# Performance work log

Hardware: AMD Instinct MI355X
Metric: run time of the kernel (lower is better)

Reference implementation:

```python
import jax, jax.numpy as jnp
import numpy as np

H = 1024      # hidden_dim
NH = 16       # num_heads
HD = H // NH  # head_dim
FF = 4096     # ff_dim
EPS = 1e-6


def layer_norm(x, gamma, beta):
    # faithful to source: unbiased std (ddof=1), divide by (std + eps)
    mean = jnp.mean(x, axis=-1, keepdims=True)
    var = jnp.sum((x - mean) ** 2, axis=-1, keepdims=True) / (x.shape[-1] - 1)
    std = jnp.sqrt(var)
    return gamma * (x - mean) / (std + EPS) + beta


def linear_mulbias(x, W, b):
    # source LinearLayer: einsum('...i,io,o->...o') -> (x @ W) * b (bias MULTIPLIES)
    return jnp.einsum('bti,io->bto', x, W) * b


def setup_inputs() -> dict:
    key = jax.random.key(0)
    ks = jax.random.split(key, 11)
    B, T = 2, 2048
    return {
        'x':      jax.random.normal(ks[0], (B, T, H), jnp.float32),
        'Wqkv':   jax.random.normal(ks[1], (H, 3 * H), jnp.float32),
        'bqkv':   jax.random.normal(ks[2], (3 * H,), jnp.float32),
        'W1':     jax.random.normal(ks[3], (H, FF), jnp.float32),
        'b1':     jax.random.normal(ks[4], (FF,), jnp.float32),
        'W2':     jax.random.normal(ks[5], (FF, H), jnp.float32),
        'b2':     jax.random.normal(ks[6], (H,), jnp.float32),
        'gamma1': jax.random.normal(ks[7], (H,), jnp.float32),
        'beta1':  jax.random.normal(ks[8], (H,), jnp.float32),
        'gamma2': jax.random.normal(ks[9], (H,), jnp.float32),
        'beta2':  jax.random.normal(ks[10], (H,), jnp.float32),
    }


def attention(x, Wqkv, bqkv):
    B, T, _ = x.shape
    qkv = linear_mulbias(x, Wqkv, bqkv)                 # [B,T,3H]
    # einops 'b t (d k h) -> k b h t d' with k=3, h=NH: last dim decomposes (d,3,h)
    qkv = qkv.reshape(B, T, HD, 3, NH)
    qkv = jnp.transpose(qkv, (3, 0, 4, 1, 2))           # [3,B,NH,T,HD]
    q, k, v = qkv[0], qkv[1], qkv[2]
    scores = jnp.einsum('bhid,bhjd->bhij', q, k) / (H ** 0.5)  # scale by full hidden_dim
    attn = jax.nn.softmax(scores, axis=-1)
    out = jnp.einsum('bhij,bhjd->bhid', attn, v)        # [B,NH,T,HD]
    return jnp.transpose(out, (0, 2, 1, 3)).reshape(B, T, H)


def reference(x, Wqkv, bqkv, W1, b1, W2, b2, gamma1, beta1, gamma2, beta2):
    # dropout is identity in eval mode
    out = layer_norm(x + attention(x, Wqkv, bqkv), gamma1, beta1)
    ffn = linear_mulbias(jnp.maximum(linear_mulbias(out, W1, b1), 0.0), W2, b2)
    out = layer_norm(out + ffn, gamma2, beta2)
    return out
```

## Files before the change

kernel.cpp:

```cpp
#include <hip/hip_runtime.h>
#include <math.h>

#define B 2
#define T 2048
#define H 1024
#define NH 16
#define HD 64
#define FF 4096
#define M_TOK (B*T)
#define LOG2E 1.4426950408889634f

typedef unsigned short u16;
typedef __attribute__((ext_vector_type(8))) short bf16x8;
typedef __attribute__((ext_vector_type(4))) float f32x4;

#define WAITBAR3  asm volatile("s_waitcnt vmcnt(3)\n\ts_barrier" ::: "memory")
#define WAITBAR4  asm volatile("s_waitcnt vmcnt(4)\n\ts_barrier" ::: "memory")
#define WAITBAR0  asm volatile("s_waitcnt vmcnt(0)\n\ts_barrier" ::: "memory")

__device__ __forceinline__ u16 f2bf(float f) {
  union { float f; unsigned u; } v; v.f = f;
  const unsigned r = (v.u + 0x7FFFu + ((v.u >> 16) & 1u)) >> 16;
  return (u16)r;
}
__device__ __forceinline__ float bf2f(u16 h) {
  union { unsigned u; float f; } v; v.u = ((unsigned)h) << 16;
  return v.f;
}
__device__ __forceinline__ unsigned cvt_pk_bf16(float lo, float hi) {
  unsigned r;
  asm("v_cvt_pk_bf16_f32 %0, %1, %2" : "=v"(r) : "v"(lo), "v"(hi));
  return r;
}
__device__ __forceinline__ float m3(float a, float b, float c) {
  return fmaxf(fmaxf(a, b), c);
}
__device__ __forceinline__ void gload16(const u16* g, u16* l) {
  __builtin_amdgcn_global_load_lds(
      (const __attribute__((address_space(1))) unsigned int*)g,
      (__attribute__((address_space(3))) unsigned int*)l, 16, 0, 0);
}

__device__ __forceinline__ int colperm(int c) {
  const int d = c / 48;
  const int rem = c - d * 48;
  return ((rem >> 4) << 10) | ((rem & 15) << 6) | d;
}

__global__ __launch_bounds__(256) void preprocess(
    const float* __restrict__ x, u16* __restrict__ xh, u16* __restrict__ xl,
    const float* __restrict__ Wqkv, u16* __restrict__ WqTh, u16* __restrict__ WqTl,
    const float* __restrict__ W1_, u16* __restrict__ W1T_,
    const float* __restrict__ W2_, u16* __restrict__ W2T_,
    const float* __restrict__ bqkv, float* __restrict__ bqkvP)
{
  const int bid = blockIdx.x;
  const int tid = threadIdx.x;
  if (bid == 6912) {
#pragma unroll
    for (int it = 0; it < 12; ++it) {
      const int c = it * 256 + tid;
      bqkvP[colperm(c)] = bqkv[c];
    }
    return;
  }
  if (bid < 4096) {
    const size_t i = ((size_t)bid * 256 + tid) * 4;
    const float4 v = *(const float4*)(x + i);
    union { u16 s[4]; uint2 u; } h, l;
    const float f[4] = {v.x, v.y, v.z, v.w};
#pragma unroll
    for (int j = 0; j < 4; ++j) {
      const u16 hb = f2bf(f[j]); h.s[j] = hb; l.s[j] = f2bf(f[j] - bf2f(hb));
    }
    *(uint2*)(xh + i) = h.u;
    *(uint2*)(xl + i) = l.u;
    return;
  }
  __shared__ float tile[64][69];
  const float* in; u16* oh; u16* ol = nullptr;
  int K, N, k0, n0, split = 0, permq = 0;
  if (bid < 4864) {
    const int tb = bid - 4096;
    in = Wqkv; oh = WqTh; ol = WqTl; K = H; N = 3*H; split = 1; permq = 1;
    n0 = (tb % 48) * 64; k0 = (tb / 48) * 64;
  } else if (bid < 5888) {
    const int tb = bid - 4864;
    in = W1_; oh = W1T_; K = H; N = FF;
    n0 = (tb & 63) * 64; k0 = (tb >> 6) * 64;
  } else {
    const int tb = bid - 5888;
    in = W2_; oh = W2T_; K = FF; N = H;
    n0 = (tb & 15) * 64; k0 = (tb >> 4) * 64;
  }
  const int r = tid >> 4, c4 = (tid & 15) * 4;
#pragma unroll
  for (int i = 0; i < 4; ++i) {
    const float4 v = *(const float4*)(in + (size_t)(k0 + i*16 + r) * N + n0 + c4);
    tile[i*16+r][c4]   = v.x; tile[i*16+r][c4+1] = v.y;
    tile[i*16+r][c4+2] = v.z; tile[i*16+r][c4+3] = v.w;
  }
  __syncthreads();
  const int n = tid >> 2, kq = tid & 3;
  union { u16 s[8]; int4 v; } ph0, ph1, pl0, pl1;
#pragma unroll
  for (int j = 0; j < 8; ++j) {
    const float f0 = tile[kq*16 + j][n];
    const float f1 = tile[kq*16 + 8 + j][n];
    const u16 h0 = f2bf(f0), h1 = f2bf(f1);
    ph0.s[j] = h0; ph1.s[j] = h1;
    if (split) { pl0.s[j] = f2bf(f0 - bf2f(h0)); pl1.s[j] = f2bf(f1 - bf2f(h1)); }
  }
  int orow = n0 + n;
  if (permq) orow = colperm(orow);
  u16* po = oh + (size_t)orow * K + k0 + kq * 16;
  *(int4*)po = ph0.v; *(int4*)(po + 8) = ph1.v;
  if (split) {
    u16* pl = ol + (size_t)orow * K + k0 + kq * 16;
    *(int4*)pl = pl0.v; *(int4*)(pl + 8) = pl1.v;
  }
}

__device__ __forceinline__ int swz(int r, int kq) {
  return r * 32 + ((kq ^ ((r >> 1) & 3)) * 8);
}

template<int RELU, int OBF>
__global__ __launch_bounds__(256) void mfma_gemm(
    const u16* __restrict__ Ah, const u16* __restrict__ Bh,
    const float* __restrict__ bias,
    float* __restrict__ Cf, u16* __restrict__ Cb,
    int M, int N, int K)
{
  __shared__ u16 lds[24576];
  const int tid = threadIdx.x;
  const int bid = blockIdx.x;
  const int xcd = bid & 7;
  const int idx = bid >> 3;
  const int row0 = (xcd * 4 + (idx & 3)) * 128;
  const int col0 = (idx >> 2) * 128;
  const int wv = tid >> 6, lane = tid & 63;
  const int wr = wv >> 1, wc = wv & 1;
  const int kq = lane >> 4, fr = lane & 15;

  f32x4 acc[4][4] = {};

#define GSTAGE(lbase, gb, rowbase, kk) do { \
    _Pragma("unroll") \
    for (int t_ = 0; t_ < 2; ++t_) { \
      const int c_ = wv * 2 + t_; \
      const int idx_ = c_ * 64 + lane; \
      const int r_ = idx_ >> 2; \
      const int kq_ = (idx_ & 3) ^ ((r_ >> 1) & 3); \
      gload16((gb) + (size_t)((rowbase) + r_) * K + (kk) + kq_ * 8, \
              &lds[(lbase) + c_ * 512]); \
    } } while (0)

  const int nk = K >> 5;
  GSTAGE(0, Ah, row0, 0);            GSTAGE(4096, Bh, col0, 0);
  GSTAGE(8192, Ah, row0, 32);        GSTAGE(8192 + 4096, Bh, col0, 32);
  WAITBAR4;
  int cslot = 0, islot = 2;
  for (int i = 0; i < nk; ++i) {
    if (i + 2 < nk) {
      const int kk = (i + 2) * 32;
      GSTAGE(islot * 8192, Ah, row0, kk);
      GSTAGE(islot * 8192 + 4096, Bh, col0, kk);
      islot = (islot == 2) ? 0 : islot + 1;
    }
    const int rb = cslot * 8192;
    bf16x8 a_h[4];
#pragma unroll
    for (int m = 0; m < 4; ++m)
      a_h[m] = *(const bf16x8*)&lds[rb + swz(wr*64 + m*16 + fr, kq)];
#pragma unroll
    for (int n = 0; n < 4; ++n) {
      const bf16x8 b_h = *(const bf16x8*)&lds[rb + 4096 + swz(wc*64 + n*16 + fr, kq)];
#pragma unroll
      for (int m = 0; m < 4; ++m)
        acc[m][n] = __builtin_amdgcn_mfma_f32_16x16x32_bf16(a_h[m], b_h, acc[m][n], 0, 0, 0);
    }
    cslot = (cslot == 2) ? 0 : cslot + 1;
    if (i + 1 < nk) { if (i + 2 < nk) WAITBAR4; else WAITBAR0; }
  }
#undef GSTAGE

  const int orow0 = row0 + wr * 64, ocol0 = col0 + wc * 64;
#pragma unroll
  for (int n = 0; n < 4; ++n) {
    const int col = ocol0 + n * 16 + fr;
    const float bs = bias[col];
#pragma unroll
    for (int m = 0; m < 4; ++m) {
      const int rbase = orow0 + m * 16 + kq * 4;
#pragma unroll
      for (int j = 0; j < 4; ++j) {
        float v = acc[m][n][j] * bs;
        if (RELU) v = fmaxf(v, 0.0f);
        const size_t off = (size_t)(rbase + j) * N + col;
        if (OBF) Cb[off] = f2bf(v); else Cf[off] = v;
      }
    }
  }
}

__global__ __launch_bounds__(256) void mfma_qkv(
    const u16* __restrict__ Ah, const u16* __restrict__ Al,
    const u16* __restrict__ Bh, const u16* __restrict__ Bl,
    const float* __restrict__ biasP,
    u16* __restrict__ Qh, u16* __restrict__ Ql,
    u16* __restrict__ Kh, u16* __restrict__ Kl, u16* __restrict__ VT)
{
  const int K = H;
  __shared__ u16 lds[32768];
  const int tid = threadIdx.x;
  const int bid = blockIdx.x;
  const int xcd = bid & 7;
  const int idx = bid >> 3;
  const int row0 = (xcd * 4 + (idx & 3)) * 128;
  const int col0 = (idx >> 2) * 128;
  const int wv = tid >> 6, lane = tid & 63;
  const int wr = wv >> 1, wc = wv & 1;
  const int kq = lane >> 4, fr = lane & 15;
  const bool isV = (col0 >= 2048);

  f32x4 acc[4][4] = {};

#define QSTAGE(lbase, gb, rowbase, kk) do { \
    _Pragma("unroll") \
    for (int t_ = 0; t_ < 2; ++t_) { \
      const int c_ = wv * 2 + t_; \
      const int idx_ = c_ * 64 + lane; \
      const int r_ = idx_ >> 2; \
      const int kq_ = (idx_ & 3) ^ ((r_ >> 1) & 3); \
      gload16((gb) + (size_t)((rowbase) + r_) * K + (kk) + kq_ * 8, \
              &lds[(lbase) + c_ * 512]); \
    } } while (0)

  QSTAGE(0, Ah, row0, 0);
  QSTAGE(4096, Bh, col0, 0);
  if (!isV) { QSTAGE(8192, Al, row0, 0); QSTAGE(12288, Bl, col0, 0); }
  __syncthreads();

  int cur = 0;
  for (int k0 = 0; k0 < K; k0 += 32) {
    const int nxt = cur ^ 1;
    if (k0 + 32 < K) {
      QSTAGE(nxt*16384, Ah, row0, k0 + 32);
      QSTAGE(nxt*16384 + 4096, Bh, col0, k0 + 32);
      if (!isV) { QSTAGE(nxt*16384 + 8192, Al, row0, k0 + 32);
                  QSTAGE(nxt*16384 + 12288, Bl, col0, k0 + 32); }
    }
    const int rb = cur * 16384;
    bf16x8 a_h[4], a_l[4];
#pragma unroll
    for (int m = 0; m < 4; ++m) {
      a_h[m] = *(const bf16x8*)&lds[rb + swz(wr*64 + m*16 + fr, kq)];
      if (!isV) a_l[m] = *(const bf16x8*)&lds[rb + 8192 + swz(wr*64 + m*16 + fr, kq)];
    }
#pragma unroll
    for (int n = 0; n < 4; ++n) {
      const bf16x8 b_h = *(const bf16x8*)&lds[rb + 4096 + swz(wc*64 + n*16 + fr, kq)];
#pragma unroll
      for (int m = 0; m < 4; ++m)
        acc[m][n] = __builtin_amdgcn_mfma_f32_16x16x32_bf16(a_h[m], b_h, acc[m][n], 0, 0, 0);
      if (!isV) {
        const bf16x8 b_l = *(const bf16x8*)&lds[rb + 12288 + swz(wc*64 + n*16 + fr, kq)];
#pragma unroll
        for (int m = 0; m < 4; ++m) {
          acc[m][n] = __builtin_amdgcn_mfma_f32_16x16x32_bf16(a_h[m], b_l, acc[m][n], 0, 0, 0);
          acc[m][n] = __builtin_amdgcn_mfma_f32_16x16x32_bf16(a_l[m], b_h, acc[m][n], 0, 0, 0);
        }
      }
    }
    __syncthreads();
    cur = nxt;
  }
#undef QSTAGE

  const float qscale = LOG2E / 32.0f;
  const int orow0 = row0 + wr * 64, ocol0 = col0 + wc * 64;
  const int kcls = col0 >> 10;

  if (kcls == 2) {
#pragma unroll
    for (int n = 0; n < 4; ++n) {
      const int dc = wc * 64 + n * 16 + fr;
      const float bs = biasP[ocol0 + n * 16 + fr];
#pragma unroll
      for (int m = 0; m < 4; ++m) {
        const int trb = wr * 64 + m * 16 + kq * 4;
#pragma unroll
        for (int j = 0; j < 4; ++j)
          lds[dc * 132 + trb + j] = f2bf(acc[m][n][j] * bs);
      }
    }
    __syncthreads();
    const int dr_ = tid >> 1, half = tid & 1;
    const int hh = ((col0 >> 6) & 15) + (dr_ >> 6);
    const int d = dr_ & 63;
    const int b = row0 >> 11, t0r = row0 & (T - 1);
    u16* dstp = VT + (((size_t)(b * NH + hh)) * HD + d) * T + t0r + half * 64;
    const int sbase = dr_ * 132 + half * 64;
#pragma unroll
    for (int q = 0; q < 8; ++q) {
      union { uint2 u2[2]; int4 v; } pkv;
      pkv.u2[0] = *(const uint2*)&lds[sbase + q * 8];
      pkv.u2[1] = *(const uint2*)&lds[sbase + q * 8 + 4];
      *(int4*)(dstp + q * 8) = pkv.v;
    }
    return;
  }

#pragma unroll
  for (int n = 0; n < 4; ++n) {
    const int colp = ocol0 + n * 16 + fr;
    const int d = colp & 63, hh = (colp >> 6) & 15;
    const float bs = biasP[colp];
#pragma unroll
    for (int m = 0; m < 4; ++m) {
      const int rbase = orow0 + m * 16 + kq * 4;
#pragma unroll
      for (int j = 0; j < 4; ++j) {
        const int row = rbase + j;
        const int b = row >> 11, t = row & (T - 1);
        const size_t dst = (((size_t)(b * NH + hh)) * T + t) * HD + d;
        float v = acc[m][n][j] * bs;
        if (kcls == 0) {
          v *= qscale;
          const u16 hb = f2bf(v);
          Qh[dst] = hb; Ql[dst] = f2bf(v - bf2f(hb));
        } else {
          const u16 hb = f2bf(v);
          Kh[dst] = hb; Kl[dst] = f2bf(v - bf2f(hb));
        }
      }
    }
  }
}

__global__ __launch_bounds__(512, 2) void mfma_ffn2(
    const u16* __restrict__ Ah, const u16* __restrict__ Bh,
    const u16* __restrict__ Res, const float* __restrict__ bias,
    float* __restrict__ Y)
{
  const int N = H, K = FF;
  __shared__ u16 lds[2 * 24576];
  const int tid = threadIdx.x;
  const int bid = blockIdx.x;
  const int xcd = bid & 7;
  const int idx = bid >> 3;
  const int row0 = (xcd * 4 + (idx & 3)) * 128;
  const int col0 = (idx >> 2) * 128;
  const int wv8 = tid >> 6, lane = tid & 63;
  const int grp = wv8 >> 2, wv = wv8 & 3;
  const int wr = wv >> 1, wc = wv & 1;
  const int kq = lane >> 4, fr = lane & 15;
  const int kb = grp * (K >> 1);
  u16* gl = &lds[grp * 24576];

  f32x4 acc[4][4] = {};

#define GSTAGE2(lbase, gb, rowbase, kk) do { \
    _Pragma("unroll") \
    for (int t_ = 0; t_ < 2; ++t_) { \
      const int c_ = wv * 2 + t_; \
      const int idx_ = c_ * 64 + lane; \
      const int r_ = idx_ >> 2; \
      const int kq_ = (idx_ & 3) ^ ((r_ >> 1) & 3); \
      gload16((gb) + (size_t)((rowbase) + r_) * K + (kk) + kq_ * 8, \
              &gl[(lbase) + c_ * 512]); \
    } } while (0)

  const int nk = (K >> 1) >> 5;
  GSTAGE2(0, Ah, row0, kb);            GSTAGE2(4096, Bh, col0, kb);
  GSTAGE2(8192, Ah, row0, kb + 32);    GSTAGE2(8192 + 4096, Bh, col0, kb + 32);
  WAITBAR4;
  int cslot = 0, islot = 2;
  for (int i = 0; i < nk; ++i) {
    if (i + 2 < nk) {
      const int kk = kb + (i + 2) * 32;
      GSTAGE2(islot * 8192, Ah, row0, kk);
      GSTAGE2(islot * 8192 + 4096, Bh, col0, kk);
      islot = (islot == 2) ? 0 : islot + 1;
    }
    const int rb = cslot * 8192;
    bf16x8 a_h[4];
#pragma unroll
    for (int m = 0; m < 4; ++m)
      a_h[m] = *(const bf16x8*)&gl[rb + swz(wr*64 + m*16 + fr, kq)];
#pragma unroll
    for (int n = 0; n < 4; ++n) {
      const bf16x8 b_h = *(const bf16x8*)&gl[rb + 4096 + swz(wc*64 + n*16 + fr, kq)];
#pragma unroll
      for (int m = 0; m < 4; ++m)
        acc[m][n] = __builtin_amdgcn_mfma_f32_16x16x32_bf16(a_h[m], b_h, acc[m][n], 0, 0, 0);
    }
    cslot = (cslot == 2) ? 0 : cslot + 1;
    if (i + 1 < nk) { if (i + 2 < nk) WAITBAR4; else WAITBAR0; }
  }
#undef GSTAGE2

  __syncthreads();
  float* fm = (float*)lds;
  const int base = wv * 4096;
  if (grp == 1) {
#pragma unroll
    for (int m = 0; m < 4; ++m)
#pragma unroll
      for (int n = 0; n < 4; ++n)
        *(f32x4*)&fm[base + (m*4 + n)*256 + lane*4] = acc[m][n];
  }
  __syncthreads();
  if (grp == 0) {
    const int orow0 = row0 + wr * 64, ocol0 = col0 + wc * 64;
#pragma unroll
    for (int n = 0; n < 4; ++n) {
      const int col = ocol0 + n * 16 + fr;
      const float bs = bias[col];
#pragma unroll
      for (int m = 0; m < 4; ++m) {
        const f32x4 ob = *(const f32x4*)&fm[base + (m*4 + n)*256 + lane*4];
        const int rbase = orow0 + m * 16 + kq * 4;
#pragma unroll
        for (int j = 0; j < 4; ++j) {
          const size_t off = (size_t)(rbase + j) * N + col;
          Y[off] = bf2f(Res[off]) + (acc[m][n][j] + ob[j]) * bs;
        }
      }
    }
  }
}

__device__ __forceinline__ int sigma_k(int r) {
  return ((r >> 5) << 5) | (((r >> 2) & 3) << 3) | (((r >> 4) & 1) << 2) | (r & 3);
}

__global__ __launch_bounds__(512, 4) void flash_attn_mfma(
    const u16* __restrict__ Qh, const u16* __restrict__ Ql,
    const u16* __restrict__ Kh, const u16* __restrict__ Kl,
    const u16* __restrict__ VT, float* __restrict__ Out)
{
  __shared__ u16 sm[3 * 12288];
  const int i = blockIdx.x;
  const int slot = i >> 3;
  const int bh = (i & 7) * 4 + (slot >> 4);
  const int row0 = (slot & 15) * 128;
  const int b = bh >> 4, h = bh & 15;
  const int tid = threadIdx.x, wave = tid >> 6, lane = tid & 63;
  const int fr = lane & 15, kq = lane >> 4;

  bf16x8 qh[2], ql[2];
  const size_t qoff = ((size_t)bh * T + row0 + wave*16 + fr) * HD + kq*8;
#pragma unroll
  for (int ks = 0; ks < 2; ++ks) {
    qh[ks] = *(const bf16x8*)(Qh + qoff + ks*32);
    ql[ks] = *(const bf16x8*)(Ql + qoff + ks*32);
  }

  bf16x8 ones8;
#pragma unroll
  for (int z = 0; z < 8; ++z) ones8[z] = (short)0x3F80;

  f32x4 o[4] = {};
  f32x4 oex = {};
  float m_ = -1e30f;

  const int c_ = wave;
  const int r0_ = c_ * 8 + (lane >> 3), s_ = lane & 7;
  const int cd0 = s_ ^ (r0_ & 7);
  const int k0_ = sigma_k(r0_);
  const u16* pKh0 = Kh + ((size_t)bh*T + k0_)*HD + cd0*8;
  const u16* pKl0 = Kl + ((size_t)bh*T + k0_)*HD + cd0*8;
  const u16* pV0  = VT + ((size_t)bh*HD + r0_)*T + cd0*8;

#define FSTAGE(sb) do { \
    gload16(pKh0, &sm[(sb) + c_*512]); \
    gload16(pKl0, &sm[(sb) + 4096 + c_*512]); \
    gload16(pV0,  &sm[(sb) + 8192 + c_*512]); \
    pKh0 += 64*HD; pKl0 += 64*HD; pV0 += 64; \
  } while (0)

  FSTAGE(0);
  FSTAGE(12288);
  WAITBAR3;
  int cslot = 0, islot = 2;

  const int NT = T / 64;
  for (int t = 0; t < NT; ++t) {
    if (t + 2 < NT) {
      FSTAGE(islot * 12288);
      islot = (islot == 2) ? 0 : islot + 1;
    }
    const u16* smb = &sm[cslot * 12288];

    f32x4 s[4] = {};
    __builtin_amdgcn_s_setprio(1);
#pragma unroll
    for (int ks = 0; ks < 2; ++ks) {
#pragma unroll
      for (int n = 0; n < 4; ++n) {
        const int kr = n * 16 + fr;
        const int sl = ((ks*4 + kq) ^ (kr & 7)) * 8;
        const bf16x8 kh_ = *(const bf16x8*)&smb[kr*64 + sl];
        const bf16x8 kl_ = *(const bf16x8*)&smb[4096 + kr*64 + sl];
        s[n] = __builtin_amdgcn_mfma_f32_16x16x32_bf16(kh_, qh[ks], s[n], 0, 0, 0);
        s[n] = __builtin_amdgcn_mfma_f32_16x16x32_bf16(kl_, qh[ks], s[n], 0, 0, 0);
        s[n] = __builtin_amdgcn_mfma_f32_16x16x32_bf16(kh_, ql[ks], s[n], 0, 0, 0);
      }
    }
    __builtin_amdgcn_s_setprio(0);

    const float g0 = m3(s[0][0], s[0][1], s[0][2]);
    const float g1 = m3(s[0][3], s[1][0], s[1][1]);
    const float g2 = m3(s[1][2], s[1][3], s[2][0]);
    const float g3 = m3(s[2][1], s[2][2], s[2][3]);
    const float g4 = m3(s[3][0], s[3][1], s[3][2]);
    float mx = fmaxf(m3(g0, g1, g2), m3(g3, g4, s[3][3]));
    mx = fmaxf(mx, __shfl_xor(mx, 16));
    mx = fmaxf(mx, __shfl_xor(mx, 32));
    if (!__all(mx <= m_ + 8.0f)) {
      const float mn = fmaxf(m_, mx);
      const float fsc = exp2f(m_ - mn);
      m_ = mn;
#pragma unroll
      for (int n = 0; n < 4; ++n) {
        o[n][0] *= fsc; o[n][1] *= fsc;
        o[n][2] *= fsc; o[n][3] *= fsc;
      }
      oex[0] *= fsc; oex[1] *= fsc; oex[2] *= fsc; oex[3] *= fsc;
    }

    float p[4][4];
#pragma unroll
    for (int n = 0; n < 4; ++n)
#pragma unroll
      for (int jj = 0; jj < 4; ++jj)
        p[n][jj] = exp2f(s[n][jj] - m_);

    unsigned pk[4][2];
#pragma unroll
    for (int n = 0; n < 4; ++n) {
      pk[n][0] = cvt_pk_bf16(p[n][0], p[n][1]);
      pk[n][1] = cvt_pk_bf16(p[n][2], p[n][3]);
    }

    __builtin_amdgcn_s_setprio(1);
#pragma unroll
    for (int ks = 0; ks < 2; ++ks) {
      union { unsigned u[4]; bf16x8 v; } pb;
      pb.u[0] = pk[2*ks][0];   pb.u[1] = pk[2*ks][1];
      pb.u[2] = pk[2*ks+1][0]; pb.u[3] = pk[2*ks+1][1];
#pragma unroll
      for (int n = 0; n < 4; ++n) {
        const int dr = n * 16 + fr;
        const bf16x8 vf = *(const bf16x8*)&smb[8192 + dr*64 + (((ks*4 + kq) ^ (dr & 7)) * 8)];
        o[n] = __builtin_amdgcn_mfma_f32_16x16x32_bf16(vf, pb.v, o[n], 0, 0, 0);
      }
      oex = __builtin_amdgcn_mfma_f32_16x16x32_bf16(ones8, pb.v, oex, 0, 0, 0);
    }
    __builtin_amdgcn_s_setprio(0);

    cslot = (cslot == 2) ? 0 : cslot + 1;
    if (t + 1 < NT) { if (t + 2 < NT) WAITBAR3; else WAITBAR0; }
  }
#undef FSTAGE

  {
    const float inv = 1.0f / oex[0];
    const size_t qrow = (size_t)b * T + row0 + wave*16 + fr;
#pragma unroll
    for (int n = 0; n < 4; ++n) {
      float4 ov;
      ov.x = o[n][0] * inv; ov.y = o[n][1] * inv;
      ov.z = o[n][2] * inv; ov.w = o[n][3] * inv;
      *(float4*)(Out + qrow * H + h * HD + n * 16 + kq * 4) = ov;
    }
  }
}

__global__ __launch_bounds__(256) void ln_residual(
    const float* __restrict__ A, const float* __restrict__ Bz,
    const float* __restrict__ gamma, const float* __restrict__ beta,
    u16* __restrict__ obf)
{
  const int row = blockIdx.x, tid = threadIdx.x;
  const int wave = tid >> 6, lane = tid & 63;
  const size_t off = (size_t)row * H + tid * 4;
  const float4 av = *(const float4*)(A + off);
  const float4 bv = *(const float4*)(Bz + off);
  float4 y; y.x = av.x + bv.x; y.y = av.y + bv.y; y.z = av.z + bv.z; y.w = av.w + bv.w;
  float s  = y.x + y.y + y.z + y.w;
  float ss = y.x*y.x + y.y*y.y + y.z*y.z + y.w*y.w;
#pragma unroll
  for (int o = 32; o >= 1; o >>= 1) { s += __shfl_xor(s, o); ss += __shfl_xor(ss, o); }
  __shared__ float red[2][4];
  if (lane == 0) { red[0][wave] = s; red[1][wave] = ss; }
  __syncthreads();
  s  = red[0][0] + red[0][1] + red[0][2] + red[0][3];
  ss = red[1][0] + red[1][1] + red[1][2] + red[1][3];
  const float mean = s * (1.0f / (float)H);
  float var = (ss - (float)H * mean * mean) * (1.0f / (float)(H - 1));
  var = fmaxf(var, 0.0f);
  const float inv = 1.0f / (sqrtf(var) + 1e-6f);
  const float4 gv = *(const float4*)(gamma + tid * 4);
  const float4 be = *(const float4*)(beta + tid * 4);
  float4 o;
  o.x = gv.x * (y.x - mean) * inv + be.x;
  o.y = gv.y * (y.y - mean) * inv + be.y;
  o.z = gv.z * (y.z - mean) * inv + be.z;
  o.w = gv.w * (y.w - mean) * inv + be.w;
  union { u16 s[4]; uint2 u; } pk;
  pk.s[0] = f2bf(o.x); pk.s[1] = f2bf(o.y); pk.s[2] = f2bf(o.z); pk.s[3] = f2bf(o.w);
  *(uint2*)(obf + off) = pk.u;
}

__global__ __launch_bounds__(256) void ln_only(
    const float* __restrict__ Yv,
    const float* __restrict__ gamma, const float* __restrict__ beta,
    float* __restrict__ out)
{
  const int row = blockIdx.x, tid = threadIdx.x;
  const int wave = tid >> 6, lane = tid & 63;
  const size_t off = (size_t)row * H + tid * 4;
  const float4 y = *(const float4*)(Yv + off);
  float s  = y.x + y.y + y.z + y.w;
  float ss = y.x*y.x + y.y*y.y + y.z*y.z + y.w*y.w;
#pragma unroll
  for (int o = 32; o >= 1; o >>= 1) { s += __shfl_xor(s, o); ss += __shfl_xor(ss, o); }
  __shared__ float red[2][4];
  if (lane == 0) { red[0][wave] = s; red[1][wave] = ss; }
  __syncthreads();
  s  = red[0][0] + red[0][1] + red[0][2] + red[0][3];
  ss = red[1][0] + red[1][1] + red[1][2] + red[1][3];
  const float mean = s * (1.0f / (float)H);
  float var = (ss - (float)H * mean * mean) * (1.0f / (float)(H - 1));
  var = fmaxf(var, 0.0f);
  const float inv = 1.0f / (sqrtf(var) + 1e-6f);
  const float4 gv = *(const float4*)(gamma + tid * 4);
  const float4 be = *(const float4*)(beta + tid * 4);
  float4 o;
  o.x = gv.x * (y.x - mean) * inv + be.x;
  o.y = gv.y * (y.y - mean) * inv + be.y;
  o.z = gv.z * (y.z - mean) * inv + be.z;
  o.w = gv.w * (y.w - mean) * inv + be.w;
  *(float4*)(out + off) = o;
}

extern "C" void kernel_launch(void* const* d_in, const int* in_sizes, int n_in,
                              void* d_out, int out_size, void* d_ws, size_t ws_size,
                              hipStream_t stream)
{
  const float* x    = (const float*)d_in[0];
  const float* Wqkv = (const float*)d_in[1];
  const float* bqkv = (const float*)d_in[2];
  const float* W1   = (const float*)d_in[3];
  const float* b1   = (const float*)d_in[4];
  const float* W2   = (const float*)d_in[5];
  const float* b2   = (const float*)d_in[6];
  const float* g1   = (const float*)d_in[7];
  const float* be1  = (const float*)d_in[8];
  const float* g2   = (const float*)d_in[9];
  const float* be2  = (const float*)d_in[10];
  float* out = (float*)d_out;
  char* w = (char*)d_ws;

  u16*   Qh    = (u16*)  (w + 0);
  u16*   Ql    = (u16*)  (w + 8388608);
  u16*   Khb   = (u16*)  (w + 16777216);
  u16*   Klb   = (u16*)  (w + 25165824);
  u16*   VTb   = (u16*)  (w + 41943040);
  u16*   h1b   = (u16*)  (w + 0);
  u16*   xh    = (u16*)  (w + 52428800);
  u16*   xl    = (u16*)  (w + 60817408);
  u16*   WqTh  = (u16*)  (w + 69206016);
  u16*   WqTl  = (u16*)  (w + 75497472);
  float* attn  = (float*)(w + 102760448);
  float* Yb    = (float*)(w + 102760448);
  u16*   W1T   = (u16*)  (w + 119537664);
  u16*   W2T   = (u16*)  (w + 127926272);
  u16*   ln1b  = (u16*)  (w + 136314880);
  float* bqkvP = (float*)(w + 144703488);

  preprocess<<<6913, 256, 0, stream>>>(x, xh, xl, Wqkv, WqTh, WqTl,
                                       W1, W1T, W2, W2T, bqkv, bqkvP);
  mfma_qkv<<<24 * 32, 256, 0, stream>>>(xh, xl, WqTh, WqTl, bqkvP,
                                        Qh, Ql, Khb, Klb, VTb);
  flash_attn_mfma<<<512, 512, 0, stream>>>(Qh, Ql, Khb, Klb, VTb, attn);
  ln_residual<<<M_TOK, 256, 0, stream>>>(x, attn, g1, be1, ln1b);
  mfma_gemm<1,1><<<32 * 32, 256, 0, stream>>>(ln1b, W1T, b1,
                                              nullptr, h1b, M_TOK, FF, H);
  mfma_ffn2<<<256, 512, 0, stream>>>(h1b, W2T, ln1b, b2, Yb);
  ln_only<<<M_TOK, 256, 0, stream>>>(Yb, g2, be2, out);
}
```

Baseline: 260.9 us.

## Triple-buffer V-block QKV GEMM and store FFN2 output in bf16

V column blocks of the QKV GEMM, which use only the high bf16 part, now get their own loop with a three-slot LDS ring buffer, two tiles of prefetch and vmcnt-based waits instead of full syncs. The Q/K path keeps the double-buffered hi/lo loop without the per-iteration isV branches. Separately, the FFN2 output is written as bf16 instead of fp32 and read back as bf16 by the final layernorm, halving that intermediate traffic but losing precision before the last layernorm.

New measurement: 261.5 us. About the same (+0.2%).

```diff
diff --git a/kernel.cpp b/kernel.cpp
--- a/kernel.cpp
+++ b/kernel.cpp
@@ -237,52 +237,37 @@
               &lds[(lbase) + c_ * 512]); \
     } } while (0)
 
-  QSTAGE(0, Ah, row0, 0);
-  QSTAGE(4096, Bh, col0, 0);
-  if (!isV) { QSTAGE(8192, Al, row0, 0); QSTAGE(12288, Bl, col0, 0); }
-  __syncthreads();
-
-  int cur = 0;
-  for (int k0 = 0; k0 < K; k0 += 32) {
-    const int nxt = cur ^ 1;
-    if (k0 + 32 < K) {
-      QSTAGE(nxt*16384, Ah, row0, k0 + 32);
-      QSTAGE(nxt*16384 + 4096, Bh, col0, k0 + 32);
-      if (!isV) { QSTAGE(nxt*16384 + 8192, Al, row0, k0 + 32);
-                  QSTAGE(nxt*16384 + 12288, Bl, col0, k0 + 32); }
-    }
-    const int rb = cur * 16384;
-    bf16x8 a_h[4], a_l[4];
-#pragma unroll
-    for (int m = 0; m < 4; ++m) {
-      a_h[m] = *(const bf16x8*)&lds[rb + swz(wr*64 + m*16 + fr, kq)];
-      if (!isV) a_l[m] = *(const bf16x8*)&lds[rb + 8192 + swz(wr*64 + m*16 + fr, kq)];
-    }
-#pragma unroll
-    for (int n = 0; n < 4; ++n) {
-      const bf16x8 b_h = *(const bf16x8*)&lds[rb + 4096 + swz(wc*64 + n*16 + fr, kq)];
+  if (isV) {
+    const int nk = K >> 5;
+    QSTAGE(0, Ah, row0, 0);            QSTAGE(4096, Bh, col0, 0);
+    QSTAGE(8192, Ah, row0, 32);        QSTAGE(8192 + 4096, Bh, col0, 32);
+    WAITBAR4;
+    int cslot = 0, islot = 2;
+    for (int i = 0; i < nk; ++i) {
+      if (i + 2 < nk) {
+        const int kk = (i + 2) * 32;
+        QSTAGE(islot * 8192, Ah, row0, kk);
+        QSTAGE(islot * 8192 + 4096, Bh, col0, kk);
+        islot = (islot == 2) ? 0 : islot + 1;
+      }
+      const int rb = cslot * 8192;
+      bf16x8 a_h[4];
 #pragma unroll
       for (int m = 0; m < 4; ++m)
-        acc[m][n] = __builtin_amdgcn_mfma_f32_16x16x32_bf16(a_h[m], b_h, acc[m][n], 0, 0, 0);
-      if (!isV) {
-        const bf16x8 b_l = *(const bf16x8*)&lds[rb + 12288 + swz(wc*64 + n*16 + fr, kq)];
-#pragma unroll
-        for (int m = 0; m < 4; ++m) {
-          acc[m][n] = __builtin_amdgcn_mfma_f32_16x16x32_bf16(a_h[m], b_l, acc[m][n], 0, 0, 0);
-          acc[m][n] = __builtin_amdgcn_mfma_f32_16x16x32_bf16(a_l[m], b_h, acc[m][n], 0, 0, 0);
-        }
-      }
+        a_h[m] = *(const bf16x8*)&lds[rb + swz(wr*64 + m*16 + fr, kq)];
+#pragma unroll
+      for (int n = 0; n < 4; ++n) {
+        const bf16x8 b_h = *(const bf16x8*)&lds[rb + 4096 + swz(wc*64 + n*16 + fr, kq)];
+#pragma unroll
+        for (int m = 0; m < 4; ++m)
+          acc[m][n] = __builtin_amdgcn_mfma_f32_16x16x32_bf16(a_h[m], b_h, acc[m][n], 0, 0, 0);
+      }
+      cslot = (cslot == 2) ? 0 : cslot + 1;
+      if (i + 1 < nk) { if (i + 2 < nk) WAITBAR4; else WAITBAR0; }
     }
     __syncthreads();
-    cur = nxt;
-  }
-#undef QSTAGE
-
-  const float qscale = LOG2E / 32.0f;
-  const int orow0 = row0 + wr * 64, ocol0 = col0 + wc * 64;
-  const int kcls = col0 >> 10;
-
-  if (kcls == 2) {
+
+    const int ocol0 = col0 + wc * 64;
 #pragma unroll
     for (int n = 0; n < 4; ++n) {
       const int dc = wc * 64 + n * 16 + fr;
@@ -312,6 +297,47 @@
     return;
   }
 
+  QSTAGE(0, Ah, row0, 0);
+  QSTAGE(4096, Bh, col0, 0);
+  QSTAGE(8192, Al, row0, 0);
+  QSTAGE(12288, Bl, col0, 0);
+  __syncthreads();
+
+  int cur = 0;
+  for (int k0 = 0; k0 < K; k0 += 32) {
+    const int nxt = cur ^ 1;
+    if (k0 + 32 < K) {
+      QSTAGE(nxt*16384, Ah, row0, k0 + 32);
+      QSTAGE(nxt*16384 + 4096, Bh, col0, k0 + 32);
+      QSTAGE(nxt*16384 + 8192, Al, row0, k0 + 32);
+      QSTAGE(nxt*16384 + 12288, Bl, col0, k0 + 32);
+    }
+    const int rb = cur * 16384;
+    bf16x8 a_h[4], a_l[4];
+#pragma unroll
+    for (int m = 0; m < 4; ++m) {
+      a_h[m] = *(const bf16x8*)&lds[rb + swz(wr*64 + m*16 + fr, kq)];
+      a_l[m] = *(const bf16x8*)&lds[rb + 8192 + swz(wr*64 + m*16 + fr, kq)];
+    }
+#pragma unroll
+    for (int n = 0; n < 4; ++n) {
+      const bf16x8 b_h = *(const bf16x8*)&lds[rb + 4096 + swz(wc*64 + n*16 + fr, kq)];
+      const bf16x8 b_l = *(const bf16x8*)&lds[rb + 12288 + swz(wc*64 + n*16 + fr, kq)];
+#pragma unroll
+      for (int m = 0; m < 4; ++m) {
+        acc[m][n] = __builtin_amdgcn_mfma_f32_16x16x32_bf16(a_h[m], b_h, acc[m][n], 0, 0, 0);
+        acc[m][n] = __builtin_amdgcn_mfma_f32_16x16x32_bf16(a_h[m], b_l, acc[m][n], 0, 0, 0);
+        acc[m][n] = __builtin_amdgcn_mfma_f32_16x16x32_bf16(a_l[m], b_h, acc[m][n], 0, 0, 0);
+      }
+    }
+    __syncthreads();
+    cur = nxt;
+  }
+#undef QSTAGE
+
+  const float qscale = LOG2E / 32.0f;
+  const int orow0 = row0 + wr * 64, ocol0 = col0 + wc * 64;
+  const int kcls = col0 >> 10;
 #pragma unroll
   for (int n = 0; n < 4; ++n) {
     const int colp = ocol0 + n * 16 + fr;
@@ -342,7 +368,7 @@
 __global__ __launch_bounds__(512, 2) void mfma_ffn2(
     const u16* __restrict__ Ah, const u16* __restrict__ Bh,
     const u16* __restrict__ Res, const float* __restrict__ bias,
-    float* __restrict__ Y)
+    u16* __restrict__ Y)
 {
   const int N = H, K = FF;
   __shared__ u16 lds[2 * 24576];
@@ -425,7 +451,7 @@
 #pragma unroll
         for (int j = 0; j < 4; ++j) {
           const size_t off = (size_t)(rbase + j) * N + col;
-          Y[off] = bf2f(Res[off]) + (acc[m][n][j] + ob[j]) * bs;
+          Y[off] = f2bf(bf2f(Res[off]) + (acc[m][n][j] + ob[j]) * bs);
         }
       }
     }
@@ -616,14 +642,18 @@
 }
 
 __global__ __launch_bounds__(256) void ln_only(
-    const float* __restrict__ Yv,
+    const u16* __restrict__ Yv,
     const float* __restrict__ gamma, const float* __restrict__ beta,
     float* __restrict__ out)
 {
   const int row = blockIdx.x, tid = threadIdx.x;
   const int wave = tid >> 6, lane = tid & 63;
   const size_t off = (size_t)row * H + tid * 4;
-  const float4 y = *(const float4*)(Yv + off);
+  union { uint2 u; u16 s[4]; } yu;
+  yu.u = *(const uint2*)(Yv + off);
+  float4 y;
+  y.x = bf2f(yu.s[0]); y.y = bf2f(yu.s[1]);
+  y.z = bf2f(yu.s[2]); y.w = bf2f(yu.s[3]);
   float s  = y.x + y.y + y.z + y.w;
   float ss = y.x*y.x + y.y*y.y + y.z*y.z + y.w*y.w;
 #pragma unroll
@@ -676,7 +706,7 @@
   u16*   WqTh  = (u16*)  (w + 69206016);
   u16*   WqTl  = (u16*)  (w + 75497472);
   float* attn  = (float*)(w + 102760448);
-  float* Yb    = (float*)(w + 102760448);
+  u16*   Yb    = (u16*)  (w + 102760448);
   u16*   W1T   = (u16*)  (w + 119537664);
   u16*   W2T   = (u16*)  (w + 127926272);
   u16*   ln1b  = (u16*)  (w + 136314880);
```
